# Kernel tuning notes

Hardware: AMD Instinct MI355X
Metric: run time of the kernel (lower is better)

Reference implementation:

```python
import jax, jax.numpy as jnp
import numpy as np

B, T, C, U = 256, 1024, 128, 100   # batch, time, num_classes (incl. blank), max label len
BLANK = C - 1                      # TF/Keras CTC: blank is the LAST class
NEG = -1.0e30                      # log-space -inf surrogate (fp32-safe)
EPS = 1e-7                         # keras backend epsilon used in ctc_batch_cost


def setup_inputs() -> dict:
    key = jax.random.key(0)
    k1, k2, k3 = jax.random.split(key, 3)
    # ctc_batch_cost consumes post-softmax probabilities
    logits = jax.random.normal(k1, (B, T, C), dtype=jnp.float32)
    y_pred = jax.nn.softmax(logits, axis=-1)
    y_true = jax.random.randint(k2, (B, U), 0, BLANK)          # labels in [0, C-2]
    label_len = jax.random.randint(k3, (B,), 1, U + 1)         # 1..U
    return {"y_pred": y_pred, "y_true": y_true, "label_len": label_len}


def _ctc_batch_cost(y_pred, y_true, label_len):
    # log probs, matching keras: log(prob + epsilon)
    logp = jnp.log(y_pred + EPS)                               # [B,T,C]
    S = 2 * U + 1
    # extended label sequence: blank, l1, blank, l2, ..., blank
    ext = jnp.full((B, S), BLANK, dtype=y_true.dtype)
    ext = ext.at[:, 1::2].set(y_true)                          # [B,S]
    # skip (s-2 -> s) allowed iff ext[s] != blank and ext[s] != ext[s-2]
    can_skip = jnp.concatenate(
        [jnp.zeros((B, 2), dtype=bool),
         (ext[:, 2:] != BLANK) & (ext[:, 2:] != ext[:, :-2])], axis=1)  # [B,S]

    logp_t = jnp.transpose(logp, (1, 0, 2))                    # [T,B,C]
    # t = 0 init: only s=0 (blank) and s=1 (first label) reachable
    lp0 = jnp.take_along_axis(logp_t[0], ext, axis=1)          # [B,S]
    alpha0 = jnp.full((B, S), NEG, dtype=logp.dtype)
    alpha0 = alpha0.at[:, 0].set(lp0[:, 0]).at[:, 1].set(lp0[:, 1])

    def step(alpha, lp_c):
        # lp_c: [B,C] log probs at time t; gather per extended-label position
        lp = jnp.take_along_axis(lp_c, ext, axis=1)            # [B,S]
        a1 = jnp.pad(alpha[:, :-1], ((0, 0), (1, 0)), constant_values=NEG)
        a2 = jnp.pad(alpha[:, :-2], ((0, 0), (2, 0)), constant_values=NEG)
        a2 = jnp.where(can_skip, a2, NEG)
        alpha = jax.nn.logsumexp(jnp.stack([alpha, a1, a2]), axis=0) + lp
        return alpha, None

    alpha, _ = jax.lax.scan(step, alpha0, logp_t[1:])          # [B,S]
    # total log-likelihood ends at s = 2L-1 (last label) or s = 2L (trailing blank)
    end = 2 * label_len[:, None]                               # [B,1]
    a_end = jnp.take_along_axis(alpha, jnp.concatenate([end - 1, end], axis=1), axis=1)
    return -jax.nn.logsumexp(a_end, axis=1, keepdims=True)     # [B,1] per-example loss


def reference(y_pred, y_true, label_len):
    # matches tf.keras.backend.ctc_batch_cost(y_true, y_pred, fill(T), label_len)
    return _ctc_batch_cost(y_pred, y_true, label_len)
```

## Files before the change

kernel.cpp:

```cpp
#include <hip/hip_runtime.h>


#define Bc 256
#define Tc 1024
#define Cc 128
#define Uc 100
#define BLANKc 127
#define EPSc 1e-7f
#define PF 16
#define LN2f 0.69314718055994530942f

__global__ __launch_bounds__(64) void ctc_lin_kernel(
    const float* __restrict__ y_pred,
    const int*   __restrict__ y_true,
    const int*   __restrict__ label_len,
    float*       __restrict__ out)
{
    __shared__ float shA[204];
    __shared__ int   shE[64];

    const int b    = blockIdx.x;
    const int lane = threadIdx.x;
    const float* gp = y_pred + (size_t)b * (Tc * Cc);

    const int k0  = 2 * lane, k1 = 2 * lane + 1;
    const int k0c = k0 < Uc ? k0 : Uc - 1;
    const int k1c = k1 < Uc ? k1 : Uc - 1;
    const int y0  = y_true[b * Uc + k0c];
    const int y1  = y_true[b * Uc + k1c];
    int ym1 = y0;
    if (lane > 0) ym1 = y_true[b * Uc + k0 - 1];
    const float ms1 = (lane > 0 && y0 != ym1) ? 1.0f : 0.0f;
    const float ms3 = (y1 != y0) ? 1.0f : 0.0f;
    const float mh  = (lane > 0) ? 1.0f : 0.0f;

    float a0 = 0.0f, a1 = 0.0f, a2 = 0.0f, a3 = 0.0f;
    if (lane == 0) {
        a0 = gp[BLANKc] + EPSc;
        a1 = gp[y0] + EPSc;
    }
    int e = 0;

    float fB[PF], fL0[PF], fL1[PF];
    {
        const float* q = gp + Cc;
#pragma unroll
        for (int j = 0; j < PF; ++j) {
            fB[j]  = q[j * Cc + BLANKc];
            fL0[j] = q[j * Cc + y0];
            fL1[j] = q[j * Cc + y1];
        }
    }

    auto step = [&](float pbr, float p0r, float p1r) {
        const int   el  = __shfl_up(e, 1, 64);
        const float h1r = __shfl_up(a3, 1, 64);
        int d = el - e; d = d > 126 ? 126 : d;
        const float h1 = mh * ldexpf(h1r, d);
        const float pb = pbr + EPSc, p0 = p0r + EPSc, p1 = p1r + EPSc;
        const float n0 = (a0 + h1) * pb;
        const float n1 = (a1 + a0 + ms1 * h1) * p0;
        const float n2 = (a2 + a1) * pb;
        const float n3 = (a3 + a2 + ms3 * a1) * p1;
        a0 = n0; a1 = n1; a2 = n2; a3 = n3;
        const float sm = (a0 + a1) + (a2 + a3);
        if (!(sm > 0.0f)) e = el;
    };

    auto renorm = [&]() {
        const float m = fmaxf(fmaxf(a0, a1), fmaxf(a2, a3));
        int ex = (int)((__float_as_uint(m) >> 23) & 0xFF) - 127;
        ex = (m > 0.0f) ? ex : 0;
        a0 = ldexpf(a0, -ex); a1 = ldexpf(a1, -ex);
        a2 = ldexpf(a2, -ex); a3 = ldexpf(a3, -ex);
        e += ex;
    };

    const float* nxt = gp + (size_t)(1 + PF) * Cc;
    for (int c = 0; c < 62; ++c) {
#pragma unroll
        for (int j = 0; j < PF; ++j) {
            const float pb = fB[j], p0 = fL0[j], p1 = fL1[j];
            fB[j]  = nxt[j * Cc + BLANKc];
            fL0[j] = nxt[j * Cc + y0];
            fL1[j] = nxt[j * Cc + y1];
            step(pb, p0, p1);
            if ((j & 3) == 3) renorm();
        }
        nxt += PF * Cc;
    }
#pragma unroll
    for (int j = 0; j < PF; ++j) {
        const float pb = fB[j], p0 = fL0[j], p1 = fL1[j];
        if (j < PF - 1) {
            fB[j]  = nxt[j * Cc + BLANKc];
            fL0[j] = nxt[j * Cc + y0];
            fL1[j] = nxt[j * Cc + y1];
        }
        step(pb, p0, p1);
        if ((j & 3) == 3) renorm();
    }
#pragma unroll
    for (int j = 0; j < PF - 1; ++j) {
        step(fB[j], fL0[j], fL1[j]);
        if ((j & 3) == 3) renorm();
    }

    if (lane < 51) {
        shA[4 * lane + 0] = a0; shA[4 * lane + 1] = a1;
        shA[4 * lane + 2] = a2; shA[4 * lane + 3] = a3;
        shE[lane] = e;
    }
    __syncthreads();
    if (lane == 0) {
        const int L  = label_len[b];
        const int s1 = 2 * L - 1, s2 = 2 * L;
        const float v1 = shA[s1], v2 = shA[s2];
        const int   e1 = shE[s1 >> 2], e2 = shE[s2 >> 2];
        const int   em = e1 > e2 ? e1 : e2;
        const float sum = ldexpf(v1, e1 - em) + ldexpf(v2, e2 - em);
        const float r   = __log2f(sum) + (float)em;
        out[b] = -LN2f * r;
    }
}

extern "C" void kernel_launch(void* const* d_in, const int* in_sizes, int n_in,
                              void* d_out, int out_size, void* d_ws, size_t ws_size,
                              hipStream_t stream) {
    const float* y_pred    = (const float*)d_in[0];
    const int*   y_true    = (const int*)d_in[1];
    const int*   label_len = (const int*)d_in[2];
    float*       out       = (float*)d_out;
    ctc_lin_kernel<<<Bc, 64, 0, stream>>>(y_pred, y_true, label_len, out);
}
```

Before: 291.8 us.

## Skew CTC recurrence across lanes with LDS row ring buffer

Restructures the time recurrence as a wavefront: lane i processes time step n-i, so the cross-lane dependency comes from the previous iteration's shuffle instead of a same-step shuffle. This takes the shuffle latency off the serial critical path. Probability rows are staged through a 128-slot LDS ring buffer filled with coalesced float2 loads held in a small register queue, replacing scattered per-lane global gathers. The cost is about 63 extra skewed drain steps, a 66KB LDS buffer that limits occupancy, and subtle LDS ordering across lanes with no barriers, relying on wave-synchronous execution.

```diff
diff --git a/kernel.cpp b/kernel.cpp
--- a/kernel.cpp
+++ b/kernel.cpp
@@ -7,15 +7,18 @@
 #define Uc 100
 #define BLANKc 127
 #define EPSc 1e-7f
-#define PF 16
 #define LN2f 0.69314718055994530942f
+#define RSTRIDE 130
+#define NSLOT 128
+#define QD 8
 
-__global__ __launch_bounds__(64) void ctc_lin_kernel(
+__global__ __launch_bounds__(64) void ctc_skew_kernel(
     const float* __restrict__ y_pred,
     const int*   __restrict__ y_true,
     const int*   __restrict__ label_len,
     float*       __restrict__ out)
 {
+    __shared__ float rowbuf[NSLOT * RSTRIDE];
     __shared__ float shA[204];
     __shared__ int   shE[64];
 
@@ -23,102 +26,102 @@
     const int lane = threadIdx.x;
     const float* gp = y_pred + (size_t)b * (Tc * Cc);
 
-    const int k0  = 2 * lane, k1 = 2 * lane + 1;
-    const int k0c = k0 < Uc ? k0 : Uc - 1;
-    const int k1c = k1 < Uc ? k1 : Uc - 1;
-    const int y0  = y_true[b * Uc + k0c];
-    const int y1  = y_true[b * Uc + k1c];
+    const int k0  = 2*lane, k1 = 2*lane+1;
+    const int k0c = k0 < Uc ? k0 : Uc-1;
+    const int k1c = k1 < Uc ? k1 : Uc-1;
+    const int y0  = y_true[b*Uc + k0c];
+    const int y1  = y_true[b*Uc + k1c];
     int ym1 = y0;
-    if (lane > 0) ym1 = y_true[b * Uc + k0 - 1];
+    if (lane > 0) ym1 = y_true[b*Uc + k0 - 1];
     const float ms1 = (lane > 0 && y0 != ym1) ? 1.0f : 0.0f;
     const float ms3 = (y1 != y0) ? 1.0f : 0.0f;
     const float mh  = (lane > 0) ? 1.0f : 0.0f;
 
-    float a0 = 0.0f, a1 = 0.0f, a2 = 0.0f, a3 = 0.0f;
-    if (lane == 0) {
-        a0 = gp[BLANKc] + EPSc;
-        a1 = gp[y0] + EPSc;
-    }
+    float a0=0.f, a1=0.f, a2=0.f, a3=0.f;
+    if (lane == 0) { a0 = gp[BLANKc]+EPSc; a1 = gp[y0]+EPSc; }
     int e = 0;
 
-    float fB[PF], fL0[PF], fL1[PF];
-    {
-        const float* q = gp + Cc;
 #pragma unroll
-        for (int j = 0; j < PF; ++j) {
-            fB[j]  = q[j * Cc + BLANKc];
-            fL0[j] = q[j * Cc + y0];
-            fL1[j] = q[j * Cc + y1];
-        }
+    for (int i = 0; i < 8; ++i) {
+        const int f4  = i*64 + lane;
+        const int row = f4 >> 5;
+        const int c4  = (f4 & 31) * 4;
+        const float4 v = *(const float4*)(gp + row*Cc + c4);
+        float* dst = &rowbuf[row*RSTRIDE + c4];
+        dst[0]=v.x; dst[1]=v.y; dst[2]=v.z; dst[3]=v.w;
     }
 
-    auto step = [&](float pbr, float p0r, float p1r) {
-        const int   el  = __shfl_up(e, 1, 64);
-        const float h1r = __shfl_up(a3, 1, 64);
+    float2 Q[QD];
+#pragma unroll
+    for (int k = 0; k < QD; ++k)
+        Q[k] = *(const float2*)(gp + (16+k)*Cc + lane*2);
+
+    float q2a = 0.f, q1a = 0.f;
+    int   q2e = 0,   q1e = 0;
+
+    auto body = [&](int n, int j, bool fzp) {
+        const int rr = n - lane;
+        const int rc = (rr < 0 ? 0 : rr) & (NSLOT-1);
+        const float* rowp = &rowbuf[rc * RSTRIDE];
+        const float pbr = rowp[BLANKc];
+        const float p0r = rowp[y0];
+        const float p1r = rowp[y1];
+        const int j8 = (n-1) & (QD-1);
+        const int ws = (n+15) & (NSLOT-1);
+        *(float2*)&rowbuf[ws*RSTRIDE + lane*2] = Q[j8];
+        int lr = n+23; lr = lr > Tc-1 ? Tc-1 : lr;
+        Q[j8] = *(const float2*)(gp + lr*Cc + lane*2);
+        const float h1r = q2a; const int el = q2e;
+        q2a = q1a; q2e = q1e;
         int d = el - e; d = d > 126 ? 126 : d;
         const float h1 = mh * ldexpf(h1r, d);
         const float pb = pbr + EPSc, p0 = p0r + EPSc, p1 = p1r + EPSc;
         const float n0 = (a0 + h1) * pb;
-        const float n1 = (a1 + a0 + ms1 * h1) * p0;
+        const float n1 = (a1 + a0 + ms1*h1) * p0;
         const float n2 = (a2 + a1) * pb;
-        const float n3 = (a3 + a2 + ms3 * a1) * p1;
-        a0 = n0; a1 = n1; a2 = n2; a3 = n3;
-        const float sm = (a0 + a1) + (a2 + a3);
-        if (!(sm > 0.0f)) e = el;
+        const float n3 = (a3 + a2 + ms3*a1) * p1;
+        const float sm = (n0+n1)+(n2+n3);
+        const int   en = (sm > 0.0f) ? e : el;
+        bool upd = true;
+        if (fzp) upd = (lane >= n - (Tc-1));
+        if (upd) { a0=n0; a1=n1; a2=n2; a3=n3; e=en; }
+        if ((j & 3) == 3) {
+            const float m = fmaxf(fmaxf(a0,a1), fmaxf(a2,a3));
+            int ex = (int)((__float_as_uint(m) >> 23) & 0xFF) - 127;
+            ex = (m > 0.0f) ? ex : 0;
+            a0 = ldexpf(a0,-ex); a1 = ldexpf(a1,-ex);
+            a2 = ldexpf(a2,-ex); a3 = ldexpf(a3,-ex);
+            e += ex;
+        }
+        q1a = __shfl_up(a3, 1, 64);
+        q1e = __shfl_up(e , 1, 64);
     };
 
-    auto renorm = [&]() {
-        const float m = fmaxf(fmaxf(a0, a1), fmaxf(a2, a3));
-        int ex = (int)((__float_as_uint(m) >> 23) & 0xFF) - 127;
-        ex = (m > 0.0f) ? ex : 0;
-        a0 = ldexpf(a0, -ex); a1 = ldexpf(a1, -ex);
-        a2 = ldexpf(a2, -ex); a3 = ldexpf(a3, -ex);
-        e += ex;
-    };
-
-    const float* nxt = gp + (size_t)(1 + PF) * Cc;
-    for (int c = 0; c < 62; ++c) {
+    int n = 1;
+    for (int c = 0; c < 63; ++c) {
 #pragma unroll
-        for (int j = 0; j < PF; ++j) {
-            const float pb = fB[j], p0 = fL0[j], p1 = fL1[j];
-            fB[j]  = nxt[j * Cc + BLANKc];
-            fL0[j] = nxt[j * Cc + y0];
-            fL1[j] = nxt[j * Cc + y1];
-            step(pb, p0, p1);
-            if ((j & 3) == 3) renorm();
-        }
-        nxt += PF * Cc;
+        for (int j = 0; j < 16; ++j) { body(n, j, false); ++n; }
+    }
+    for (int c = 0; c < 4; ++c) {
+#pragma unroll
+        for (int j = 0; j < 16; ++j) { body(n, j, true); ++n; }
     }
 #pragma unroll
-    for (int j = 0; j < PF; ++j) {
-        const float pb = fB[j], p0 = fL0[j], p1 = fL1[j];
-        if (j < PF - 1) {
-            fB[j]  = nxt[j * Cc + BLANKc];
-            fL0[j] = nxt[j * Cc + y0];
-            fL1[j] = nxt[j * Cc + y1];
-        }
-        step(pb, p0, p1);
-        if ((j & 3) == 3) renorm();
-    }
-#pragma unroll
-    for (int j = 0; j < PF - 1; ++j) {
-        step(fB[j], fL0[j], fL1[j]);
-        if ((j & 3) == 3) renorm();
-    }
+    for (int j = 0; j < 14; ++j) { body(n, j, true); ++n; }
 
     if (lane < 51) {
-        shA[4 * lane + 0] = a0; shA[4 * lane + 1] = a1;
-        shA[4 * lane + 2] = a2; shA[4 * lane + 3] = a3;
+        shA[4*lane+0] = a0; shA[4*lane+1] = a1;
+        shA[4*lane+2] = a2; shA[4*lane+3] = a3;
         shE[lane] = e;
     }
     __syncthreads();
     if (lane == 0) {
         const int L  = label_len[b];
-        const int s1 = 2 * L - 1, s2 = 2 * L;
+        const int s1 = 2*L - 1, s2 = 2*L;
         const float v1 = shA[s1], v2 = shA[s2];
         const int   e1 = shE[s1 >> 2], e2 = shE[s2 >> 2];
         const int   em = e1 > e2 ? e1 : e2;
-        const float sum = ldexpf(v1, e1 - em) + ldexpf(v2, e2 - em);
+        const float sum = ldexpf(v1, e1-em) + ldexpf(v2, e2-em);
         const float r   = __log2f(sum) + (float)em;
         out[b] = -LN2f * r;
     }
@@ -131,5 +134,5 @@
     const int*   y_true    = (const int*)d_in[1];
     const int*   label_len = (const int*)d_in[2];
     float*       out       = (float*)d_out;
-    ctc_lin_kernel<<<Bc, 64, 0, stream>>>(y_pred, y_true, label_len, out);
+    ctc_skew_kernel<<<Bc, 64, 0, stream>>>(y_pred, y_true, label_len, out);
 }
```

After: 267.0 us. 1.09x faster.
